# Kernel optimization log

Hardware: AMD Instinct MI355X
Metric: run time of the kernel (lower is better)

The kernel has to match this reference:

```python
import jax, jax.numpy as jnp
import numpy as np

D_HEAD = 64  # per-head dim 'd' from init_kwargs


def layer_norm(x, g, b, eps=1e-5):
    m = x.mean(-1, keepdims=True)
    v = x.var(-1, keepdims=True)  # biased var, matches torch LayerNorm
    return (x - m) / jnp.sqrt(v + eps) * g + b


def setup_inputs() -> dict:
    key = jax.random.key(0)
    ks = jax.random.split(key, 16)
    F = 512
    B, T, N = 2, 8, 1024
    s = 1.0 / np.sqrt(F)
    u = lambda k, shape: jax.random.uniform(k, shape, jnp.float32, -s, s)
    return {
        "x": jax.random.normal(ks[0], (B, T, N, F), jnp.float32),
        "Wq": u(ks[1], (F, F)), "bq": u(ks[2], (F,)),
        "Wk": u(ks[3], (F, F)), "bk": u(ks[4], (F,)),
        "Wv": u(ks[5], (F, F)), "bv": u(ks[6], (F,)),
        "ln_g": jnp.ones((F,), jnp.float32), "ln_b": jnp.zeros((F,), jnp.float32),
        "W1": u(ks[7], (F, F)), "b1": u(ks[8], (F,)),
        "W2": u(ks[9], (F, F)), "b2": u(ks[10], (F,)),
        "lnff_g": jnp.ones((F,), jnp.float32), "lnff_b": jnp.zeros((F,), jnp.float32),
    }


def reference(x, Wq, bq, Wk, bk, Wv, bv, ln_g, ln_b, W1, b1, W2, b2, lnff_g, lnff_b):
    B, T, N, F = x.shape
    h = F // D_HEAD
    # q/k/v projections
    q = x @ Wq + bq
    k = x @ Wk + bk
    v = x @ Wv + bv
    # split last dim into heads (split+cat(dim=0) in torch == head axis here)
    qh = q.reshape(B, T, N, h, D_HEAD)
    kh = k.reshape(B, T, N, h, D_HEAD)
    vh = v.reshape(B, T, N, h, D_HEAD)
    # attention over node axis N per (batch, time, head)
    A = jnp.einsum('btqhd,btkhd->bthqk', qh, kh) / jnp.sqrt(jnp.asarray(D_HEAD, x.dtype))
    A = jax.nn.softmax(A, axis=-1)
    o = jnp.einsum('bthqk,btkhd->btqhd', A, vh).reshape(B, T, N, F)
    # residual + LN
    val = layer_norm(o + x, ln_g, ln_b)
    # FFN + final LN
    ff = jax.nn.relu(val @ W1 + b1) @ W2 + b2
    return layer_norm(ff, lnff_g, lnff_b)
```

## Files before the change

kernel.cpp:

```cpp
#include <hip/hip_runtime.h>
#include <hip/hip_bf16.h>

using bf16 = __hip_bfloat16;
typedef unsigned int u32x4 __attribute__((ext_vector_type(4)));
typedef float f32x4 __attribute__((ext_vector_type(4)));
typedef __bf16 bf16x8 __attribute__((ext_vector_type(8)));

#define DEVI __device__ __forceinline__

DEVI f32x4 mfma16(u32x4 a, u32x4 b, f32x4 c) {
    return __builtin_amdgcn_mfma_f32_16x16x32_bf16(
        __builtin_bit_cast(bf16x8, a), __builtin_bit_cast(bf16x8, b), c, 0, 0, 0);
}

struct bf8 { bf16 h[8]; };

DEVI u32x4 pack8(f32x4 lo, f32x4 hi) {
    bf8 t;
#pragma unroll
    for (int i = 0; i < 4; i++) {
        t.h[i] = __float2bfloat16(lo[i]);
        t.h[4 + i] = __float2bfloat16(hi[i]);
    }
    return __builtin_bit_cast(u32x4, t);
}

DEVI unsigned trunc2(float a, float b) {
    return __builtin_amdgcn_perm(__builtin_bit_cast(unsigned, b),
                                 __builtin_bit_cast(unsigned, a), 0x07060302);
}

DEVI void async16(const bf16* g, bf16* l) {
    __builtin_amdgcn_global_load_lds(
        (const __attribute__((address_space(1))) unsigned int*)g,
        (__attribute__((address_space(3))) unsigned int*)l, 16, 0, 0);
}

__global__ __launch_bounds__(256) void prep(
    const float* __restrict__ Wq, const float* __restrict__ Wk,
    const float* __restrict__ Wv, const float* __restrict__ W1,
    const float* __restrict__ W2, const float* __restrict__ x,
    bf16* __restrict__ WT, bf16* __restrict__ xb)
{
    int b = blockIdx.x;
    if (b < 5120) {
        int w = b >> 10;
        const float* src = (w == 0) ? Wq : (w == 1) ? Wk : (w == 2) ? Wv : (w == 3) ? W1 : W2;
        int idx = (b & 1023) * 256 + threadIdx.x;
        int n = idx >> 9, kk = idx & 511;
        WT[(size_t)w * 262144 + idx] = __float2bfloat16(src[kk * 512 + n]);
    } else {
        size_t i = ((size_t)(b - 5120) * 256 + threadIdx.x) * 8;
        f32x4 lo = *(const f32x4*)&x[i];
        f32x4 hi = *(const f32x4*)&x[i + 4];
        *(u32x4*)&xb[i] = pack8(lo, hi);
    }
}

__global__ __launch_bounds__(256) void gemm_qkv(
    const bf16* __restrict__ A, const bf16* __restrict__ WT,
    const float* __restrict__ bqp, const float* __restrict__ bkp, const float* __restrict__ bvp,
    bf16* __restrict__ qb, bf16* __restrict__ kb, bf16* __restrict__ vT)
{
    __shared__ __align__(16) bf16 As[128 * 32];
    __shared__ __align__(16) bf16 Bs[128 * 32];
    const int tid = threadIdx.x;
    const int lane = tid & 63, wave = tid >> 6;
    const int wm = (wave >> 1) * 64, wn = (wave & 1) * 64;
    const int wsel = blockIdx.y >> 2;
    const int bm = blockIdx.x * 128, bn = (blockIdx.y & 3) * 128;
    const bf16* Bt = WT + (size_t)wsel * 262144;
    const float* bias = (wsel == 0) ? bqp : (wsel == 1) ? bkp : bvp;
    const int lm = lane & 15, lq = lane >> 4;

    f32x4 acc[4][4];
#pragma unroll
    for (int i = 0; i < 4; i++)
#pragma unroll
        for (int j = 0; j < 4; j++) acc[i][j] = (f32x4){0.f, 0.f, 0.f, 0.f};

    for (int k0 = 0; k0 < 512; k0 += 32) {
        __syncthreads();
#pragma unroll
        for (int p = 0; p < 2; p++) {
            int c = p * 256 + tid;
            int r = c >> 2, kc = (c & 3) * 8;
            async16(&A[(size_t)(bm + r) * 512 + k0 + kc], &As[(p * 256 + wave * 64) * 8]);
            async16(&Bt[(size_t)(bn + r) * 512 + k0 + kc], &Bs[(p * 256 + wave * 64) * 8]);
        }
        __syncthreads();
        u32x4 af[4], bfr[4];
#pragma unroll
        for (int i = 0; i < 4; i++) af[i] = *(const u32x4*)&As[(wm + i * 16 + lm) * 32 + lq * 8];
#pragma unroll
        for (int j = 0; j < 4; j++) bfr[j] = *(const u32x4*)&Bs[(wn + j * 16 + lm) * 32 + lq * 8];
#pragma unroll
        for (int i = 0; i < 4; i++)
#pragma unroll
            for (int j = 0; j < 4; j++) acc[i][j] = mfma16(af[i], bfr[j], acc[i][j]);
    }

#pragma unroll
    for (int i = 0; i < 4; i++) {
#pragma unroll
        for (int j = 0; j < 4; j++) {
            int col = bn + wn + j * 16 + lm;
            float bv = bias[col];
#pragma unroll
            for (int r = 0; r < 4; r++) {
                int row = bm + wm + i * 16 + lq * 4 + r;
                float cv = acc[i][j][r] + bv;
                if (wsel == 0) {
                    qb[(size_t)row * 512 + col] = __float2bfloat16(cv * 0.18033688f);
                } else if (wsel == 1) {
                    kb[(size_t)row * 512 + col] = __float2bfloat16(cv);
                } else {
                    int bt = row >> 10, node = row & 1023;
                    int hh = col >> 6, d = col & 63;
                    vT[((size_t)((bt * 8 + hh) * 64 + d)) * 1024 + node] = __float2bfloat16(cv);
                }
            }
        }
    }
}

template <bool RELU>
__global__ __launch_bounds__(256) void gemm_bt(
    const bf16* __restrict__ A, const bf16* __restrict__ Bt,
    const float* __restrict__ bias, bf16* __restrict__ C)
{
    __shared__ __align__(16) bf16 As[128 * 32];
    __shared__ __align__(16) bf16 Bs[128 * 32];
    const int tid = threadIdx.x;
    const int lane = tid & 63, wave = tid >> 6;
    const int wm = (wave >> 1) * 64, wn = (wave & 1) * 64;
    const int bm = blockIdx.x * 128, bn = blockIdx.y * 128;
    const int lm = lane & 15, lq = lane >> 4;

    f32x4 acc[4][4];
#pragma unroll
    for (int i = 0; i < 4; i++)
#pragma unroll
        for (int j = 0; j < 4; j++) acc[i][j] = (f32x4){0.f, 0.f, 0.f, 0.f};

    for (int k0 = 0; k0 < 512; k0 += 32) {
        __syncthreads();
#pragma unroll
        for (int p = 0; p < 2; p++) {
            int c = p * 256 + tid;
            int r = c >> 2, kc = (c & 3) * 8;
            async16(&A[(size_t)(bm + r) * 512 + k0 + kc], &As[(p * 256 + wave * 64) * 8]);
            async16(&Bt[(size_t)(bn + r) * 512 + k0 + kc], &Bs[(p * 256 + wave * 64) * 8]);
        }
        __syncthreads();
        u32x4 af[4], bfr[4];
#pragma unroll
        for (int i = 0; i < 4; i++) af[i] = *(const u32x4*)&As[(wm + i * 16 + lm) * 32 + lq * 8];
#pragma unroll
        for (int j = 0; j < 4; j++) bfr[j] = *(const u32x4*)&Bs[(wn + j * 16 + lm) * 32 + lq * 8];
#pragma unroll
        for (int i = 0; i < 4; i++)
#pragma unroll
            for (int j = 0; j < 4; j++) acc[i][j] = mfma16(af[i], bfr[j], acc[i][j]);
    }

#pragma unroll
    for (int i = 0; i < 4; i++) {
#pragma unroll
        for (int j = 0; j < 4; j++) {
            int col = bn + wn + j * 16 + lm;
            float bv = bias[col];
#pragma unroll
            for (int r = 0; r < 4; r++) {
                int row = bm + wm + i * 16 + lq * 4 + r;
                float cv = acc[i][j][r] + bv;
                if (RELU) cv = fmaxf(cv, 0.f);
                C[(size_t)row * 512 + col] = __float2bfloat16(cv);
            }
        }
    }
}

__global__ __launch_bounds__(256) void attn_kernel(
    const bf16* __restrict__ q, const bf16* __restrict__ k,
    const bf16* __restrict__ vT, float* __restrict__ o)
{
    constexpr int KP = 72;
    constexpr int VP = 72;
    __shared__ __align__(16) bf16 Ks[64 * KP];
    __shared__ __align__(16) bf16 Vs[64 * VP];
    __shared__ __align__(16) bf16 Ps[4][64 * VP];

    const int tid = threadIdx.x, lane = tid & 63, wave = tid >> 6;
    const int group = blockIdx.x;
    const int bt = group >> 3, hh = group & 7;
    const int lm = lane & 15, lq = lane >> 4;
    const int qrow0 = bt * 1024 + blockIdx.y * 256 + wave * 64;

    u32x4 qf[4][2];
#pragma unroll
    for (int tm = 0; tm < 4; tm++)
#pragma unroll
        for (int kk2 = 0; kk2 < 2; kk2++)
            qf[tm][kk2] = *(const u32x4*)&q[(size_t)(qrow0 + tm * 16 + lm) * 512 + hh * 64 + kk2 * 32 + lq * 8];

    const bf16* kbase = k + (size_t)(bt * 1024) * 512 + hh * 64;
    const bf16* vbase = vT + (size_t)group * 64 * 1024;
    bf16* Pw = &Ps[wave][0];

    const int c0 = tid, c1 = 256 + tid;
    const int r0 = c0 >> 3, e0 = (c0 & 7) * 8;
    const int r1 = c1 >> 3, e1 = (c1 & 7) * 8;

    f32x4 accO[4][4];
#pragma unroll
    for (int tm = 0; tm < 4; tm++)
#pragma unroll
        for (int tn = 0; tn < 4; tn++) accO[tm][tn] = (f32x4){0.f, 0.f, 0.f, 0.f};
    float part[4] = {0.f, 0.f, 0.f, 0.f};

    u32x4 kreg0 = *(const u32x4*)&kbase[(size_t)r0 * 512 + e0];
    u32x4 kreg1 = *(const u32x4*)&kbase[(size_t)r1 * 512 + e1];
    u32x4 vreg0 = *(const u32x4*)&vbase[(size_t)r0 * 1024 + e0];
    u32x4 vreg1 = *(const u32x4*)&vbase[(size_t)r1 * 1024 + e1];

    for (int kt = 0; kt < 16; kt++) {
        __syncthreads();
        *(u32x4*)&Ks[r0 * KP + e0] = kreg0;
        *(u32x4*)&Ks[r1 * KP + e1] = kreg1;
        *(u32x4*)&Vs[r0 * VP + e0] = vreg0;
        *(u32x4*)&Vs[r1 * VP + e1] = vreg1;
        if (kt < 15) {
            const bf16* kn = kbase + (size_t)((kt + 1) * 64) * 512;
            const bf16* vn = vbase + (kt + 1) * 64;
            kreg0 = *(const u32x4*)&kn[(size_t)r0 * 512 + e0];
            kreg1 = *(const u32x4*)&kn[(size_t)r1 * 512 + e1];
            vreg0 = *(const u32x4*)&vn[(size_t)r0 * 1024 + e0];
            vreg1 = *(const u32x4*)&vn[(size_t)r1 * 1024 + e1];
        }
        __syncthreads();

#pragma unroll
        for (int tk = 0; tk < 4; tk++) {
            u32x4 kf0 = *(const u32x4*)&Ks[(tk * 16 + lm) * KP + lq * 8];
            u32x4 kf1 = *(const u32x4*)&Ks[(tk * 16 + lm) * KP + 32 + lq * 8];
#pragma unroll
            for (int tm = 0; tm < 4; tm++) {
                f32x4 st = (f32x4){0.f, 0.f, 0.f, 0.f};
                st = mfma16(kf0, qf[tm][0], st);
                st = mfma16(kf1, qf[tm][1], st);
                float p0 = __builtin_amdgcn_exp2f(st[0]);
                float p1 = __builtin_amdgcn_exp2f(st[1]);
                float p2 = __builtin_amdgcn_exp2f(st[2]);
                float p3 = __builtin_amdgcn_exp2f(st[3]);
                part[tm] += (p0 + p1) + (p2 + p3);
                unsigned lo = trunc2(p0, p1), hi = trunc2(p2, p3);
                unsigned long long pk2 = ((unsigned long long)hi << 32) | lo;
                *(unsigned long long*)&Pw[(tm * 16 + lm) * VP + tk * 16 + lq * 4] = pk2;
            }
        }

#pragma unroll
        for (int kc = 0; kc < 2; kc++) {
            u32x4 pf[4], vf[4];
#pragma unroll
            for (int tm = 0; tm < 4; tm++)
                pf[tm] = *(const u32x4*)&Pw[(tm * 16 + lm) * VP + kc * 32 + lq * 8];
#pragma unroll
            for (int tn = 0; tn < 4; tn++)
                vf[tn] = *(const u32x4*)&Vs[(tn * 16 + lm) * VP + kc * 32 + lq * 8];
#pragma unroll
            for (int tm = 0; tm < 4; tm++)
#pragma unroll
                for (int tn = 0; tn < 4; tn++)
                    accO[tm][tn] = mfma16(pf[tm], vf[tn], accO[tm][tn]);
        }
    }

#pragma unroll
    for (int tm = 0; tm < 4; tm++) {
        part[tm] += __shfl_xor(part[tm], 16);
        part[tm] += __shfl_xor(part[tm], 32);
    }
#pragma unroll
    for (int tm = 0; tm < 4; tm++)
#pragma unroll
        for (int r = 0; r < 4; r++) {
            float l = __shfl(part[tm], lq * 4 + r);
            float linv = 1.0f / l;
#pragma unroll
            for (int tn = 0; tn < 4; tn++) {
                int row = qrow0 + tm * 16 + lq * 4 + r;
                int col = hh * 64 + tn * 16 + lm;
                o[(size_t)row * 512 + col] = accO[tm][tn][r] * linv;
            }
        }
}

template <bool AF32, bool RES, bool OF32>
__global__ __launch_bounds__(256) void ln_kernel(
    const void* __restrict__ a, const float* __restrict__ res,
    const float* __restrict__ g, const float* __restrict__ bb, void* __restrict__ out)
{
    int row = blockIdx.x * 4 + (threadIdx.x >> 6);
    int lane = threadIdx.x & 63;
    size_t base = (size_t)row * 512 + lane * 8;
    int cbase = lane * 8;

    float x8[8];
    if (AF32) {
        const float* af = (const float*)a;
        f32x4 lo = *(const f32x4*)&af[base];
        f32x4 hi = *(const f32x4*)&af[base + 4];
#pragma unroll
        for (int i = 0; i < 4; i++) { x8[i] = lo[i]; x8[4 + i] = hi[i]; }
    } else {
        bf8 av = __builtin_bit_cast(bf8, *(const u32x4*)&((const bf16*)a)[base]);
#pragma unroll
        for (int i = 0; i < 8; i++) x8[i] = __bfloat162float(av.h[i]);
    }
    if (RES) {
        f32x4 lo = *(const f32x4*)&res[base];
        f32x4 hi = *(const f32x4*)&res[base + 4];
#pragma unroll
        for (int i = 0; i < 4; i++) { x8[i] += lo[i]; x8[4 + i] += hi[i]; }
    }

    float s = 0.f, s2 = 0.f;
#pragma unroll
    for (int i = 0; i < 8; i++) { s += x8[i]; s2 += x8[i] * x8[i]; }
#pragma unroll
    for (int off = 1; off < 64; off <<= 1) {
        s += __shfl_xor(s, off);
        s2 += __shfl_xor(s2, off);
    }
    float mean = s * (1.f / 512.f);
    float var = s2 * (1.f / 512.f) - mean * mean;
    float rstd = rsqrtf(var + 1e-5f);

    f32x4 g0 = *(const f32x4*)&g[cbase], g1 = *(const f32x4*)&g[cbase + 4];
    f32x4 b0 = *(const f32x4*)&bb[cbase], b1v = *(const f32x4*)&bb[cbase + 4];
    float y[8];
#pragma unroll
    for (int i = 0; i < 4; i++) {
        y[i] = (x8[i] - mean) * rstd * g0[i] + b0[i];
        y[4 + i] = (x8[4 + i] - mean) * rstd * g1[i] + b1v[i];
    }
    if (OF32) {
        float* op = (float*)out;
        *(f32x4*)&op[base] = (f32x4){y[0], y[1], y[2], y[3]};
        *(f32x4*)&op[base + 4] = (f32x4){y[4], y[5], y[6], y[7]};
    } else {
        bf8 ov;
#pragma unroll
        for (int i = 0; i < 8; i++) ov.h[i] = __float2bfloat16(y[i]);
        *(u32x4*)&((bf16*)out)[base] = __builtin_bit_cast(u32x4, ov);
    }
}

extern "C" void kernel_launch(void* const* d_in, const int* in_sizes, int n_in,
                              void* d_out, int out_size, void* d_ws, size_t ws_size,
                              hipStream_t stream)
{
    const float* x    = (const float*)d_in[0];
    const float* Wq   = (const float*)d_in[1];
    const float* bq   = (const float*)d_in[2];
    const float* Wk   = (const float*)d_in[3];
    const float* bk   = (const float*)d_in[4];
    const float* Wv   = (const float*)d_in[5];
    const float* bv   = (const float*)d_in[6];
    const float* ln_g = (const float*)d_in[7];
    const float* ln_b = (const float*)d_in[8];
    const float* W1   = (const float*)d_in[9];
    const float* b1   = (const float*)d_in[10];
    const float* W2   = (const float*)d_in[11];
    const float* b2   = (const float*)d_in[12];
    const float* lnffg = (const float*)d_in[13];
    const float* lnffb = (const float*)d_in[14];
    float* out = (float*)d_out;

    bf16* ws = (bf16*)d_ws;
    bf16* WT = ws;
    bf16* qb = ws + 5 * 262144;
    bf16* kb = qb + 8388608;
    bf16* vT = kb + 8388608;
    bf16* vl = qb;
    bf16* f1 = kb;
    bf16* f2 = vT;
    bf16* xb = (bf16*)d_out;

    prep<<<9216, 256, 0, stream>>>(Wq, Wk, Wv, W1, W2, x, WT, xb);

    gemm_qkv<<<dim3(128, 12), 256, 0, stream>>>(xb, WT, bq, bk, bv, qb, kb, vT);

    attn_kernel<<<dim3(128, 4), 256, 0, stream>>>(qb, kb, vT, out);

    ln_kernel<true, true, false><<<4096, 256, 0, stream>>>(out, x, ln_g, ln_b, vl);

    dim3 gg(128, 4);
    gemm_bt<true> <<<gg, 256, 0, stream>>>(vl, WT + 3 * 262144, b1, f1);
    gemm_bt<false><<<gg, 256, 0, stream>>>(f1, WT + 4 * 262144, b2, f2);

    ln_kernel<false, false, true><<<4096, 256, 0, stream>>>(f2, nullptr, lnffg, lnffb, out);
}
```

Baseline: 270.6 us.

## Restructure GEMMs with register prefetch, padded LDS, K=64 tiles and packed stores

Replaces the async global-to-LDS loads in the GEMM kernels with register-staged prefetch of the next K=64 tile into padded shared memory (stride 72), which halves the barrier count and overlaps global loads with MFMA work. Swaps the MFMA operand order in the row-major outputs so that each lane holds four consecutive columns, which allows packed 8-byte bf16 stores and vectorized bias loads. The V-transpose store also writes four contiguous nodes at once. In attention, the next-tile prefetch is moved after the barrier. The trade-off is more register pressure and a larger LDS footprint per block, which may lower occupancy.

Measured after the change: 260.0 us. 1.04x faster.

```diff
diff --git a/kernel.cpp b/kernel.cpp
--- a/kernel.cpp
+++ b/kernel.cpp
@@ -25,15 +25,16 @@
     return __builtin_bit_cast(u32x4, t);
 }
 
+DEVI unsigned long long pk4(float a, float b, float c, float d) {
+    union { unsigned long long u; bf16 h[4]; } t;
+    t.h[0] = __float2bfloat16(a); t.h[1] = __float2bfloat16(b);
+    t.h[2] = __float2bfloat16(c); t.h[3] = __float2bfloat16(d);
+    return t.u;
+}
+
 DEVI unsigned trunc2(float a, float b) {
     return __builtin_amdgcn_perm(__builtin_bit_cast(unsigned, b),
                                  __builtin_bit_cast(unsigned, a), 0x07060302);
-}
-
-DEVI void async16(const bf16* g, bf16* l) {
-    __builtin_amdgcn_global_load_lds(
-        (const __attribute__((address_space(1))) unsigned int*)g,
-        (__attribute__((address_space(3))) unsigned int*)l, 16, 0, 0);
 }
 
 __global__ __launch_bounds__(256) void prep(
@@ -57,68 +58,97 @@
     }
 }
 
+#define GEMM_BODY(EPILOGUE)                                                          \
+    constexpr int SP = 72;                                                           \
+    __shared__ __align__(16) bf16 As[128 * SP];                                      \
+    __shared__ __align__(16) bf16 Bs[128 * SP];                                      \
+    const int tid = threadIdx.x;                                                     \
+    const int lane = tid & 63, wave = tid >> 6;                                      \
+    const int wm = (wave >> 1) * 64, wn = (wave & 1) * 64;                           \
+    const int lm = lane & 15, lq = lane >> 4;                                        \
+    const int sr = tid >> 3, sc = (tid & 7) * 8;             \
+    const bf16* Ap = A + (size_t)(bm + sr) * 512 + sc;                               \
+    const bf16* Bp = Bt + (size_t)(bn + sr) * 512 + sc;                              \
+    f32x4 acc[4][4];                                                                 \
+    _Pragma("unroll") for (int i = 0; i < 4; i++)                                    \
+        _Pragma("unroll") for (int j = 0; j < 4; j++)                                \
+            acc[i][j] = (f32x4){0.f, 0.f, 0.f, 0.f};                                 \
+    u32x4 ar[4], br[4];                                                              \
+    _Pragma("unroll") for (int p = 0; p < 4; p++) {                                  \
+        ar[p] = *(const u32x4*)(Ap + (size_t)p * 32 * 512);                          \
+        br[p] = *(const u32x4*)(Bp + (size_t)p * 32 * 512);                          \
+    }                                                                                \
+    for (int k0 = 0; k0 < 512; k0 += 64) {                                           \
+        __syncthreads();                                                             \
+        _Pragma("unroll") for (int p = 0; p < 4; p++) {                              \
+            *(u32x4*)&As[(p * 32 + sr) * SP + sc] = ar[p];                           \
+            *(u32x4*)&Bs[(p * 32 + sr) * SP + sc] = br[p];                           \
+        }                                                                            \
+        __syncthreads();                                                             \
+        if (k0 < 448) {      \
+            _Pragma("unroll") for (int p = 0; p < 4; p++) {                          \
+                ar[p] = *(const u32x4*)(Ap + (size_t)p * 32 * 512 + k0 + 64);        \
+                br[p] = *(const u32x4*)(Bp + (size_t)p * 32 * 512 + k0 + 64);        \
+            }                                                                        \
+        }                                                                            \
+        _Pragma("unroll") for (int h = 0; h < 2; h++) {                              \
+            u32x4 af[4], bfr[4];                                                     \
+            _Pragma("unroll") for (int i = 0; i < 4; i++)                            \
+                af[i] = *(const u32x4*)&As[(wm + i * 16 + lm) * SP + h * 32 + lq * 8]; \
+            _Pragma("unroll") for (int j = 0; j < 4; j++)                            \
+                bfr[j] = *(const u32x4*)&Bs[(wn + j * 16 + lm) * SP + h * 32 + lq * 8]; \
+            EPILOGUE##_MMA                                                           \
+        }                                                                            \
+    }
+
+#define SWAPPED_MMA                                                                  \
+    _Pragma("unroll") for (int i = 0; i < 4; i++)                                    \
+        _Pragma("unroll") for (int j = 0; j < 4; j++)                                \
+            acc[i][j] = mfma16(bfr[j], af[i], acc[i][j]);
+#define NORMAL_MMA                                                                   \
+    _Pragma("unroll") for (int i = 0; i < 4; i++)                                    \
+        _Pragma("unroll") for (int j = 0; j < 4; j++)                                \
+            acc[i][j] = mfma16(af[i], bfr[j], acc[i][j]);
+
 __global__ __launch_bounds__(256) void gemm_qkv(
     const bf16* __restrict__ A, const bf16* __restrict__ WT,
     const float* __restrict__ bqp, const float* __restrict__ bkp, const float* __restrict__ bvp,
     bf16* __restrict__ qb, bf16* __restrict__ kb, bf16* __restrict__ vT)
 {
-    __shared__ __align__(16) bf16 As[128 * 32];
-    __shared__ __align__(16) bf16 Bs[128 * 32];
-    const int tid = threadIdx.x;
-    const int lane = tid & 63, wave = tid >> 6;
-    const int wm = (wave >> 1) * 64, wn = (wave & 1) * 64;
     const int wsel = blockIdx.y >> 2;
     const int bm = blockIdx.x * 128, bn = (blockIdx.y & 3) * 128;
     const bf16* Bt = WT + (size_t)wsel * 262144;
     const float* bias = (wsel == 0) ? bqp : (wsel == 1) ? bkp : bvp;
-    const int lm = lane & 15, lq = lane >> 4;
-
-    f32x4 acc[4][4];
-#pragma unroll
-    for (int i = 0; i < 4; i++)
-#pragma unroll
-        for (int j = 0; j < 4; j++) acc[i][j] = (f32x4){0.f, 0.f, 0.f, 0.f};
-
-    for (int k0 = 0; k0 < 512; k0 += 32) {
-        __syncthreads();
-#pragma unroll
-        for (int p = 0; p < 2; p++) {
-            int c = p * 256 + tid;
-            int r = c >> 2, kc = (c & 3) * 8;
-            async16(&A[(size_t)(bm + r) * 512 + k0 + kc], &As[(p * 256 + wave * 64) * 8]);
-            async16(&Bt[(size_t)(bn + r) * 512 + k0 + kc], &Bs[(p * 256 + wave * 64) * 8]);
-        }
-        __syncthreads();
-        u32x4 af[4], bfr[4];
-#pragma unroll
-        for (int i = 0; i < 4; i++) af[i] = *(const u32x4*)&As[(wm + i * 16 + lm) * 32 + lq * 8];
-#pragma unroll
-        for (int j = 0; j < 4; j++) bfr[j] = *(const u32x4*)&Bs[(wn + j * 16 + lm) * 32 + lq * 8];
-#pragma unroll
-        for (int i = 0; i < 4; i++)
-#pragma unroll
-            for (int j = 0; j < 4; j++) acc[i][j] = mfma16(af[i], bfr[j], acc[i][j]);
-    }
-
-#pragma unroll
-    for (int i = 0; i < 4; i++) {
-#pragma unroll
-        for (int j = 0; j < 4; j++) {
-            int col = bn + wn + j * 16 + lm;
-            float bv = bias[col];
-#pragma unroll
-            for (int r = 0; r < 4; r++) {
-                int row = bm + wm + i * 16 + lq * 4 + r;
-                float cv = acc[i][j][r] + bv;
-                if (wsel == 0) {
-                    qb[(size_t)row * 512 + col] = __float2bfloat16(cv * 0.18033688f);
-                } else if (wsel == 1) {
-                    kb[(size_t)row * 512 + col] = __float2bfloat16(cv);
-                } else {
-                    int bt = row >> 10, node = row & 1023;
-                    int hh = col >> 6, d = col & 63;
-                    vT[((size_t)((bt * 8 + hh) * 64 + d)) * 1024 + node] = __float2bfloat16(cv);
-                }
+
+    if (wsel < 2) {
+        GEMM_BODY(SWAPPED)
+        const float scale = (wsel == 0) ? 0.18033688f : 1.0f;
+        bf16* dst = (wsel == 0) ? qb : kb;
+#pragma unroll
+        for (int i = 0; i < 4; i++) {
+#pragma unroll
+            for (int j = 0; j < 4; j++) {
+                int row = bm + wm + i * 16 + lm;
+                int colb = bn + wn + j * 16 + lq * 4;
+                f32x4 b4 = *(const f32x4*)&bias[colb];
+                *(unsigned long long*)&dst[(size_t)row * 512 + colb] =
+                    pk4((acc[i][j][0] + b4[0]) * scale, (acc[i][j][1] + b4[1]) * scale,
+                        (acc[i][j][2] + b4[2]) * scale, (acc[i][j][3] + b4[3]) * scale);
+            }
+        }
+    } else {
+        GEMM_BODY(NORMAL)
+#pragma unroll
+        for (int i = 0; i < 4; i++) {
+#pragma unroll
+            for (int j = 0; j < 4; j++) {
+                int col = bn + wn + j * 16 + lm;
+                float bv = bias[col];
+                int rowb = bm + wm + i * 16 + lq * 4;
+                int btq = rowb >> 10, node = rowb & 1023;
+                *(unsigned long long*)&vT[((size_t)((btq * 8 + (col >> 6)) * 64 + (col & 63))) * 1024 + node] =
+                    pk4(acc[i][j][0] + bv, acc[i][j][1] + bv,
+                        acc[i][j][2] + bv, acc[i][j][3] + bv);
             }
         }
     }
@@ -129,54 +159,22 @@
     const bf16* __restrict__ A, const bf16* __restrict__ Bt,
     const float* __restrict__ bias, bf16* __restrict__ C)
 {
-    __shared__ __align__(16) bf16 As[128 * 32];
-    __shared__ __align__(16) bf16 Bs[128 * 32];
-    const int tid = threadIdx.x;
-    const int lane = tid & 63, wave = tid >> 6;
-    const int wm = (wave >> 1) * 64, wn = (wave & 1) * 64;
     const int bm = blockIdx.x * 128, bn = blockIdx.y * 128;
-    const int lm = lane & 15, lq = lane >> 4;
-
-    f32x4 acc[4][4];
-#pragma unroll
-    for (int i = 0; i < 4; i++)
-#pragma unroll
-        for (int j = 0; j < 4; j++) acc[i][j] = (f32x4){0.f, 0.f, 0.f, 0.f};
-
-    for (int k0 = 0; k0 < 512; k0 += 32) {
-        __syncthreads();
-#pragma unroll
-        for (int p = 0; p < 2; p++) {
-            int c = p * 256 + tid;
-            int r = c >> 2, kc = (c & 3) * 8;
-            async16(&A[(size_t)(bm + r) * 512 + k0 + kc], &As[(p * 256 + wave * 64) * 8]);
-            async16(&Bt[(size_t)(bn + r) * 512 + k0 + kc], &Bs[(p * 256 + wave * 64) * 8]);
-        }
-        __syncthreads();
-        u32x4 af[4], bfr[4];
-#pragma unroll
-        for (int i = 0; i < 4; i++) af[i] = *(const u32x4*)&As[(wm + i * 16 + lm) * 32 + lq * 8];
-#pragma unroll
-        for (int j = 0; j < 4; j++) bfr[j] = *(const u32x4*)&Bs[(wn + j * 16 + lm) * 32 + lq * 8];
-#pragma unroll
-        for (int i = 0; i < 4; i++)
-#pragma unroll
-            for (int j = 0; j < 4; j++) acc[i][j] = mfma16(af[i], bfr[j], acc[i][j]);
-    }
-
+    GEMM_BODY(SWAPPED)
 #pragma unroll
     for (int i = 0; i < 4; i++) {
 #pragma unroll
         for (int j = 0; j < 4; j++) {
-            int col = bn + wn + j * 16 + lm;
-            float bv = bias[col];
-#pragma unroll
-            for (int r = 0; r < 4; r++) {
-                int row = bm + wm + i * 16 + lq * 4 + r;
-                float cv = acc[i][j][r] + bv;
-                if (RELU) cv = fmaxf(cv, 0.f);
-                C[(size_t)row * 512 + col] = __float2bfloat16(cv);
+            int row = bm + wm + i * 16 + lm;
+            int colb = bn + wn + j * 16 + lq * 4;
+            f32x4 b4 = *(const f32x4*)&bias[colb];
+            float c0 = acc[i][j][0] + b4[0], c1 = acc[i][j][1] + b4[1];
+            float c2 = acc[i][j][2] + b4[2], c3 = acc[i][j][3] + b4[3];
+            if (RELU) {
+                c0 = fmaxf(c0, 0.f); c1 = fmaxf(c1, 0.f);
+                c2 = fmaxf(c2, 0.f); c3 = fmaxf(c3, 0.f);
             }
+            *(unsigned long long*)&C[(size_t)row * 512 + colb] = pk4(c0, c1, c2, c3);
         }
     }
 }
@@ -206,11 +204,10 @@
 
     const bf16* kbase = k + (size_t)(bt * 1024) * 512 + hh * 64;
     const bf16* vbase = vT + (size_t)group * 64 * 1024;
-    bf16* Pw = &Ps[wave][0];
-
-    const int c0 = tid, c1 = 256 + tid;
-    const int r0 = c0 >> 3, e0 = (c0 & 7) * 8;
-    const int r1 = c1 >> 3, e1 = (c1 & 7) * 8;
+    bf16* Pw = Ps[wave];
+
+    const int r0 = tid >> 3, e0 = (tid & 7) * 8;
+    const int r1 = (256 + tid) >> 3, e1 = e0;
 
     f32x4 accO[4][4];
 #pragma unroll
@@ -230,6 +227,7 @@
         *(u32x4*)&Ks[r1 * KP + e1] = kreg1;
         *(u32x4*)&Vs[r0 * VP + e0] = vreg0;
         *(u32x4*)&Vs[r1 * VP + e1] = vreg1;
+        __syncthreads();
         if (kt < 15) {
             const bf16* kn = kbase + (size_t)((kt + 1) * 64) * 512;
             const bf16* vn = vbase + (kt + 1) * 64;
@@ -238,7 +236,6 @@
             vreg0 = *(const u32x4*)&vn[(size_t)r0 * 1024 + e0];
             vreg1 = *(const u32x4*)&vn[(size_t)r1 * 1024 + e1];
         }
-        __syncthreads();
 
 #pragma unroll
         for (int tk = 0; tk < 4; tk++) {
```
